# Performance work log

Measured on AMD Instinct MI355X. Metric: run time of the kernel, lower is better.

Reference implementation:

```python
import jax, jax.numpy as jnp
import numpy as np

D = 128  # head dim

def setup_inputs() -> dict:
    key = jax.random.key(0)
    k1, k2, k3, k4, k5 = jax.random.split(key, 5)
    B, N, M, C1, C2 = 4, 4096, 4096, 1024, 1024
    x = jax.random.normal(k1, (B, N, C1), dtype=jnp.float32)
    y = jax.random.normal(k2, (B, M, C2), dtype=jnp.float32)
    # Linear(c, d, bias=False): out = inp @ W where W is [c, d]
    Wq = jax.random.normal(k3, (C1, D), dtype=jnp.float32) / np.sqrt(C1)
    Wk = jax.random.normal(k4, (C2, D), dtype=jnp.float32) / np.sqrt(C2)
    Wv = jax.random.normal(k5, (C2, D), dtype=jnp.float32) / np.sqrt(C2)
    return {"x": x, "y": y, "Wq": Wq, "Wk": Wk, "Wv": Wv}

def reference(x, y, Wq, Wk, Wv):
    q = x @ Wq                               # [B, N, d]
    k = y @ Wk                               # [B, M, d]
    v = y @ Wv                               # [B, M, d]
    scale = 1.0 / jnp.sqrt(jnp.asarray(D, dtype=q.dtype))
    a = jnp.einsum('bnd,bmd->bnm', q, k) * scale
    a = jax.nn.softmax(a, axis=-1)           # softmax FIRST
    a = jnp.triu(a, k=1)                     # post-softmax causal mask (keeps strict upper)
    out = jnp.einsum('bnm,bmd->bnd', a, v)   # [B, N, d]
    return out
```

## Files before the change

kernel.cpp:

```cpp
#include <hip/hip_runtime.h>
#include <hip/hip_bf16.h>
#include <stdint.h>


typedef __attribute__((ext_vector_type(8))) __bf16    bf16x8;
typedef __attribute__((ext_vector_type(4))) float     floatx4;
typedef __attribute__((ext_vector_type(8))) uint16_t  u16x8;
typedef __attribute__((ext_vector_type(4))) uint32_t  u32x4;

#define DEVFN __device__ __forceinline__

DEVFN uint16_t f32_to_bf16(float f) {
  uint32_t u = __builtin_bit_cast(uint32_t, f);
  u += 0x7FFFu + ((u >> 16) & 1u);
  return (uint16_t)(u >> 16);
}

DEVFN uint32_t bcast(float f) { return __builtin_bit_cast(uint32_t, f); }

DEVFN uint32_t pack2_bf16(float a, float b) {
  return ((bcast(a) + 0x8000u) >> 16) | ((bcast(b) + 0x8000u) & 0xFFFF0000u);
}

DEVFN u32x4 pack_bf16_8(float4 a0, float4 a1) {
  u32x4 o;
  o[0] = pack2_bf16(a0.x, a0.y);
  o[1] = pack2_bf16(a0.z, a0.w);
  o[2] = pack2_bf16(a1.x, a1.y);
  o[3] = pack2_bf16(a1.z, a1.w);
  return o;
}

DEVFN void gl2lds16(const void* g, void* l) {
  __builtin_amdgcn_global_load_lds(
      (const __attribute__((address_space(1))) void*)g,
      (__attribute__((address_space(3))) void*)l, 16, 0, 0);
}

__global__ __launch_bounds__(256) void wt_kernel(
    const float* __restrict__ Wq, const float* __restrict__ Wk,
    const float* __restrict__ Wv, uint16_t* __restrict__ wt) {
  int tid = blockIdx.x * 256 + threadIdx.x;
  int mat = tid >> 14;
  int rem = tid & 16383;
  int n  = rem & 127;
  int k0 = rem >> 7;
  const float* W = (mat == 0) ? Wq : ((mat == 1) ? Wk : Wv);
  u16x8 v;
#pragma unroll
  for (int j = 0; j < 8; ++j) v[j] = f32_to_bf16(W[(k0 * 8 + j) * 128 + n]);
  *(u16x8*)&wt[mat * (128 * 1024) + n * 1024 + k0 * 8] = v;
}

__global__ __launch_bounds__(256, 3) void qkv_kernel(
    const float* __restrict__ x, const float* __restrict__ y,
    const uint16_t* __restrict__ wt, uint16_t* __restrict__ q,
    uint16_t* __restrict__ k, uint16_t* __restrict__ vt) {
  constexpr int AB = 8192;
  constexpr int WB = 16384;
  __shared__ __align__(16) uint8_t sA[2 * AB];
  __shared__ __align__(16) uint8_t sW[2 * WB];
  const int t = threadIdx.x;
  const int mat = blockIdx.y, rt = blockIdx.x;
  const float* A = (mat == 0) ? x : y;
  const uint16_t* Wt = wt + mat * (128 * 1024);
  const int lane = t & 63, wv = t >> 6;
  const int wr = wv >> 1, wc = wv & 1;
  const int cidx = lane & 15, quad = lane >> 4;
  const int Arow0 = rt * 64;

  const int ar  = t >> 2;
  const int acq = t & 3;
  const float* aptr = &A[(size_t)(Arow0 + ar) * 1024 + acq * 16];
  const int aw0 = ar * 128 + (((2 * acq) ^ (ar & 7)) * 16);
  const int aw1 = ar * 128 + (((2 * acq + 1) ^ (ar & 7)) * 16);

  int wsrc[4], wdst[4];
#pragma unroll
  for (int i = 0; i < 4; ++i) {
    int G = i * 256 + t;
    int n = G >> 3, g = G & 7;
    wsrc[i] = n * 1024 + ((g ^ (n & 7)) * 8);
    wdst[i] = G * 16;
  }

  floatx4 acc[2][4];
#pragma unroll
  for (int rg = 0; rg < 2; ++rg)
#pragma unroll
    for (int ng = 0; ng < 4; ++ng) acc[rg][ng] = (floatx4){0.f, 0.f, 0.f, 0.f};

  float4 f4[4], g4[4];

#pragma unroll
  for (int i = 0; i < 4; ++i)
    gl2lds16(Wt + wsrc[i], sW + wdst[i]);
#pragma unroll
  for (int j = 0; j < 4; ++j) f4[j] = *(const float4*)(aptr + j * 4);

  for (int kt = 0; kt < 16; ++kt) {
    const int cur = kt & 1, nxt = cur ^ 1;
    if (kt < 15) {
      const int kc = (kt + 1) * 64;
#pragma unroll
      for (int i = 0; i < 4; ++i)
        gl2lds16(Wt + kc + wsrc[i], sW + nxt * WB + wdst[i]);
#pragma unroll
      for (int j = 0; j < 4; ++j) g4[j] = *(const float4*)(aptr + kc + j * 4);
      __builtin_amdgcn_sched_barrier(0);
      asm volatile("s_waitcnt vmcnt(8)" ::: "memory");
    } else {
      __builtin_amdgcn_sched_barrier(0);
      asm volatile("s_waitcnt vmcnt(0)" ::: "memory");
    }
    __builtin_amdgcn_sched_barrier(0);

    *(u32x4*)(sA + cur * AB + aw0) = pack_bf16_8(f4[0], f4[1]);
    *(u32x4*)(sA + cur * AB + aw1) = pack_bf16_8(f4[2], f4[3]);
    __builtin_amdgcn_sched_barrier(0);
    asm volatile("s_waitcnt lgkmcnt(0)" ::: "memory");
    __builtin_amdgcn_s_barrier();
    __builtin_amdgcn_sched_barrier(0);

    bf16x8 af[2][2];
#pragma unroll
    for (int rg = 0; rg < 2; ++rg)
#pragma unroll
      for (int ks = 0; ks < 2; ++ks)
        af[rg][ks] = *(const bf16x8*)
            (sA + cur * AB + (wr * 32 + rg * 16 + cidx) * 128 +
             (((ks * 4 + quad) ^ (cidx & 7)) * 16));
    __builtin_amdgcn_s_setprio(1);
#pragma unroll
    for (int ng = 0; ng < 4; ++ng) {
      const int n = wc * 64 + ng * 16 + cidx;
      bf16x8 b0 = *(const bf16x8*)
          (sW + cur * WB + n * 128 + (((quad) ^ (cidx & 7)) * 16));
      bf16x8 b1 = *(const bf16x8*)
          (sW + cur * WB + n * 128 + (((4 + quad) ^ (cidx & 7)) * 16));
#pragma unroll
      for (int rg = 0; rg < 2; ++rg) {
        acc[rg][ng] = __builtin_amdgcn_mfma_f32_16x16x32_bf16(af[rg][0], b0, acc[rg][ng], 0, 0, 0);
        acc[rg][ng] = __builtin_amdgcn_mfma_f32_16x16x32_bf16(af[rg][1], b1, acc[rg][ng], 0, 0, 0);
      }
    }
    __builtin_amdgcn_s_setprio(0);
    __builtin_amdgcn_sched_barrier(0);
    asm volatile("s_waitcnt lgkmcnt(0)" ::: "memory");
    __builtin_amdgcn_s_barrier();
    __builtin_amdgcn_sched_barrier(0);

    if (kt < 15) {
#pragma unroll
      for (int j = 0; j < 4; ++j) f4[j] = g4[j];
    }
  }

  if (mat < 2) {
    uint16_t* outp = (mat == 0) ? q : k;
#pragma unroll
    for (int rg = 0; rg < 2; ++rg)
#pragma unroll
      for (int r = 0; r < 4; ++r) {
        int row = Arow0 + wr * 32 + rg * 16 + quad * 4 + r;
#pragma unroll
        for (int ng = 0; ng < 4; ++ng)
          outp[row * 128 + wc * 64 + ng * 16 + cidx] = f32_to_bf16(acc[rg][ng][r]);
      }
  } else {
    int bq = rt >> 6;
    int mbase = (rt & 63) * 64;
#pragma unroll
    for (int rg = 0; rg < 2; ++rg)
#pragma unroll
      for (int r = 0; r < 4; ++r) {
        int m = mbase + wr * 32 + rg * 16 + quad * 4 + r;
#pragma unroll
        for (int ng = 0; ng < 4; ++ng)
          vt[(size_t)(bq * 128 + wc * 64 + ng * 16 + cidx) * 4096 + m] =
              f32_to_bf16(acc[rg][ng][r]);
      }
  }
}

__global__ __launch_bounds__(256, 2) void attn_kernel(
    const uint16_t* __restrict__ q, const uint16_t* __restrict__ k,
    const uint16_t* __restrict__ vt, float* __restrict__ opart,
    float* __restrict__ lpart, int mlen, int iters) {
  constexpr int KB = 16384, VB = 16384;
  __shared__ __align__(16) uint8_t sK[2 * KB];
  __shared__ __align__(16) uint8_t sV[2 * VB];
  const int t = threadIdx.x;
  const int lane = t & 63, wv = t >> 6;
  const int cidx = lane & 15, quad = lane >> 4;
  const int qt = blockIdx.x, h = blockIdx.y, b = blockIdx.z;
  const int qmin = qt * 128 + wv * 32;
  const int mbase = h * mlen;

  const uint16_t* qb = q + (size_t)(b * 4096) * 128;
  const uint8_t* kb = (const uint8_t*)(k + (size_t)(b * 4096) * 128);
  const uint8_t* vb = (const uint8_t*)(vt + (size_t)(b * 128) * 4096);

  const float SC = 0.12751744610657223f;

  int kOffL[4], vOffL[4], kLds[4], vLds[4];
#pragma unroll
  for (int u = 0; u < 4; ++u) {
    int r  = wv * 16 + u * 4 + (lane >> 4);
    int g  = (lane & 15) ^ (r & 15);
    kOffL[u] = r * 256 + g * 16;
    kLds[u]  = (wv * 16 + u * 4) * 256;
    int rv = wv * 32 + u * 8 + (lane >> 3);
    int gv = (lane & 7) ^ (rv & 7);
    vOffL[u] = rv * 8192 + gv * 16;
    vLds[u]  = (wv * 32 + u * 8) * 128;
  }

  bf16x8 qf[2][4];
#pragma unroll
  for (int qg = 0; qg < 2; ++qg)
#pragma unroll
    for (int ks = 0; ks < 4; ++ks)
      qf[qg][ks] = *(const bf16x8*)
          &qb[(qmin + qg * 16 + cidx) * 128 + ks * 32 + quad * 8];

  floatx4 O[2][8];
#pragma unroll
  for (int qg = 0; qg < 2; ++qg)
#pragma unroll
    for (int dg = 0; dg < 8; ++dg) O[qg][dg] = (floatx4){0.f, 0.f, 0.f, 0.f};
  float lsum[2] = {0.f, 0.f};

#pragma unroll
  for (int u = 0; u < 4; ++u) {
    gl2lds16(kb + (size_t)mbase * 256 + kOffL[u], sK + kLds[u]);
    gl2lds16(vb + (size_t)mbase * 2 + vOffL[u], sV + vLds[u]);
  }
  __syncthreads();

  for (int it = 0; it < iters; ++it) {
    const int m0 = mbase + it * 64;
    const int cur = it & 1, nxt = cur ^ 1;
    if (it + 1 < iters) {
      const int m1 = m0 + 64;
#pragma unroll
      for (int u = 0; u < 4; ++u) {
        gl2lds16(kb + (size_t)m1 * 256 + kOffL[u], sK + nxt * KB + kLds[u]);
        gl2lds16(vb + (size_t)m1 * 2 + vOffL[u], sV + nxt * VB + vLds[u]);
      }
    }

    floatx4 accST[2][4];
#pragma unroll
    for (int qg = 0; qg < 2; ++qg)
#pragma unroll
      for (int ng = 0; ng < 4; ++ng) accST[qg][ng] = (floatx4){0.f, 0.f, 0.f, 0.f};
    __builtin_amdgcn_s_setprio(1);
#pragma unroll
    for (int ks = 0; ks < 4; ++ks)
#pragma unroll
      for (int ng = 0; ng < 4; ++ng) {
        bf16x8 kf = *(const bf16x8*)
            (sK + cur * KB + (ng * 16 + cidx) * 256 + ((ks * 4 + quad) ^ cidx) * 16);
        accST[0][ng] = __builtin_amdgcn_mfma_f32_16x16x32_bf16(kf, qf[0][ks], accST[0][ng], 0, 0, 0);
        accST[1][ng] = __builtin_amdgcn_mfma_f32_16x16x32_bf16(kf, qf[1][ks], accST[1][ng], 0, 0, 0);
      }
    __builtin_amdgcn_s_setprio(0);

    float p[2][4][4];
#pragma unroll
    for (int qg = 0; qg < 2; ++qg)
#pragma unroll
      for (int ng = 0; ng < 4; ++ng)
#pragma unroll
        for (int r = 0; r < 4; ++r) {
          p[qg][ng][r] = exp2f(accST[qg][ng][r] * SC);
          lsum[qg] += p[qg][ng][r];
        }

    if (m0 + 63 > qmin) {
#pragma unroll
      for (int qg = 0; qg < 2; ++qg) {
        const int base = qmin + qg * 16;
        if (m0 < base + 16) {
#pragma unroll
          for (int ng = 0; ng < 4; ++ng)
#pragma unroll
            for (int r = 0; r < 4; ++r) {
              int m = m0 + ng * 16 + quad * 4 + r;
              int n = base + cidx;
              if (m <= n) p[qg][ng][r] = 0.f;
            }
        }
      }
      uint32_t pk[2][4][2];
#pragma unroll
      for (int qg = 0; qg < 2; ++qg)
#pragma unroll
        for (int ng = 0; ng < 4; ++ng) {
          pk[qg][ng][0] = pack2_bf16(p[qg][ng][0], p[qg][ng][1]);
          pk[qg][ng][1] = pack2_bf16(p[qg][ng][2], p[qg][ng][3]);
        }
#pragma unroll
      for (int ks = 0; ks < 2; ++ks) {
        bf16x8 pbv[2];
#pragma unroll
        for (int qg = 0; qg < 2; ++qg) {
          u32x4 pbw;
#pragma unroll
          for (int j2 = 0; j2 < 4; ++j2) {
            int lr = ((quad & 1) << 3) + 2 * j2;
            int srcl = ((lr >> 2) << 4) + cidx;
            uint32_t lo = (uint32_t)__shfl((int)pk[qg][2 * ks][j2 & 1], srcl);
            uint32_t hi = (uint32_t)__shfl((int)pk[qg][2 * ks + 1][j2 & 1], srcl);
            pbw[j2] = (quad & 2) ? hi : lo;
          }
          pbv[qg] = __builtin_bit_cast(bf16x8, pbw);
        }
        __builtin_amdgcn_s_setprio(1);
#pragma unroll
        for (int dg = 0; dg < 8; ++dg) {
          bf16x8 vf = *(const bf16x8*)
              (sV + cur * VB + (dg * 16 + cidx) * 128 +
               (((ks * 4 + quad) ^ cidx) & 7) * 16);
          O[0][dg] = __builtin_amdgcn_mfma_f32_16x16x32_bf16(vf, pbv[0], O[0][dg], 0, 0, 0);
          O[1][dg] = __builtin_amdgcn_mfma_f32_16x16x32_bf16(vf, pbv[1], O[1][dg], 0, 0, 0);
        }
        __builtin_amdgcn_s_setprio(0);
      }
    }
    __syncthreads();
  }

#pragma unroll
  for (int qg = 0; qg < 2; ++qg) {
    lsum[qg] += __shfl_xor(lsum[qg], 16);
    lsum[qg] += __shfl_xor(lsum[qg], 32);
    const int n = qmin + qg * 16 + cidx;
    float* op = opart + ((size_t)h * 16384 + b * 4096 + n) * 128;
#pragma unroll
    for (int dg = 0; dg < 8; ++dg)
      *(float4*)&op[dg * 16 + quad * 4] = __builtin_bit_cast(float4, O[qg][dg]);
    if (quad == 0) lpart[h * 16384 + b * 4096 + n] = lsum[qg];
  }
}

__global__ __launch_bounds__(256) void combine_kernel(
    const float* __restrict__ opart, const float* __restrict__ lpart,
    float* __restrict__ out, int hcount) {
  size_t i = (size_t)blockIdx.x * 256 + threadIdx.x;
  size_t e = i * 4;
  int row = (int)(e >> 7);
  float4 acc = {0.f, 0.f, 0.f, 0.f};
  float l = 0.f;
  for (int h = 0; h < hcount; ++h) {
    float4 ov = *(const float4*)&opart[(size_t)h * 2097152 + e];
    acc.x += ov.x; acc.y += ov.y; acc.z += ov.z; acc.w += ov.w;
    l += lpart[h * 16384 + row];
  }
  float inv = 1.0f / l;
  float4 o;
  o.x = acc.x * inv; o.y = acc.y * inv; o.z = acc.z * inv; o.w = acc.w * inv;
  *(float4*)&out[e] = o;
}

extern "C" void kernel_launch(void* const* d_in, const int* in_sizes, int n_in,
                              void* d_out, int out_size, void* d_ws, size_t ws_size,
                              hipStream_t stream) {
  const float* x  = (const float*)d_in[0];
  const float* y  = (const float*)d_in[1];
  const float* Wq = (const float*)d_in[2];
  const float* Wk = (const float*)d_in[3];
  const float* Wv = (const float*)d_in[4];
  uint16_t* ws = (uint16_t*)d_ws;
  uint16_t* wt = ws;
  uint16_t* q  = ws + 393216;
  uint16_t* k  = q + 2097152;
  uint16_t* vt = k + 2097152;
  float* opart = (float*)((char*)d_ws + 13369344);
  int hcount = (ws_size >= (size_t)13369344 + 4 * 8454144) ? 4 : 2;
  float* lpart = opart + (size_t)hcount * 2097152;
  float* o = (float*)d_out;
  int mlen = 4096 / hcount, iters = mlen / 64;

  hipLaunchKernelGGL(wt_kernel,      dim3(192),            dim3(256), 0, stream, Wq, Wk, Wv, wt);
  hipLaunchKernelGGL(qkv_kernel,     dim3(256, 3),         dim3(256), 0, stream, x, y, wt, q, k, vt);
  hipLaunchKernelGGL(attn_kernel,    dim3(32, hcount, 4),  dim3(256), 0, stream, q, k, vt, opart, lpart, mlen, iters);
  hipLaunchKernelGGL(combine_kernel, dim3(2048),           dim3(256), 0, stream, opart, lpart, o, hcount);
}
```

Measured before the change: 230.1 us.

## Prefetch projection tiles two stages ahead through registers instead of direct LDS loads

```diff
diff --git a/kernel.cpp b/kernel.cpp
--- a/kernel.cpp
+++ b/kernel.cpp
@@ -80,8 +80,8 @@
   for (int i = 0; i < 4; ++i) {
     int G = i * 256 + t;
     int n = G >> 3, g = G & 7;
-    wsrc[i] = n * 1024 + ((g ^ (n & 7)) * 8);
-    wdst[i] = G * 16;
+    wsrc[i] = n * 1024 + g * 8;
+    wdst[i] = n * 128 + ((g ^ (n & 7)) * 16);
   }
 
   floatx4 acc[2][4];
@@ -90,71 +90,82 @@
 #pragma unroll
     for (int ng = 0; ng < 4; ++ng) acc[rg][ng] = (floatx4){0.f, 0.f, 0.f, 0.f};
 
-  float4 f4[4], g4[4];
-
-#pragma unroll
-  for (int i = 0; i < 4; ++i)
-    gl2lds16(Wt + wsrc[i], sW + wdst[i]);
-#pragma unroll
-  for (int j = 0; j < 4; ++j) f4[j] = *(const float4*)(aptr + j * 4);
-
-  for (int kt = 0; kt < 16; ++kt) {
-    const int cur = kt & 1, nxt = cur ^ 1;
-    if (kt < 15) {
-      const int kc = (kt + 1) * 64;
-#pragma unroll
-      for (int i = 0; i < 4; ++i)
-        gl2lds16(Wt + kc + wsrc[i], sW + nxt * WB + wdst[i]);
-#pragma unroll
-      for (int j = 0; j < 4; ++j) g4[j] = *(const float4*)(aptr + kc + j * 4);
-      __builtin_amdgcn_sched_barrier(0);
-      asm volatile("s_waitcnt vmcnt(8)" ::: "memory");
-    } else {
-      __builtin_amdgcn_sched_barrier(0);
-      asm volatile("s_waitcnt vmcnt(0)" ::: "memory");
-    }
-    __builtin_amdgcn_sched_barrier(0);
-
-    *(u32x4*)(sA + cur * AB + aw0) = pack_bf16_8(f4[0], f4[1]);
-    *(u32x4*)(sA + cur * AB + aw1) = pack_bf16_8(f4[2], f4[3]);
-    __builtin_amdgcn_sched_barrier(0);
-    asm volatile("s_waitcnt lgkmcnt(0)" ::: "memory");
-    __builtin_amdgcn_s_barrier();
-    __builtin_amdgcn_sched_barrier(0);
-
-    bf16x8 af[2][2];
-#pragma unroll
-    for (int rg = 0; rg < 2; ++rg)
-#pragma unroll
-      for (int ks = 0; ks < 2; ++ks)
-        af[rg][ks] = *(const bf16x8*)
-            (sA + cur * AB + (wr * 32 + rg * 16 + cidx) * 128 +
-             (((ks * 4 + quad) ^ (cidx & 7)) * 16));
-    __builtin_amdgcn_s_setprio(1);
-#pragma unroll
-    for (int ng = 0; ng < 4; ++ng) {
-      const int n = wc * 64 + ng * 16 + cidx;
-      bf16x8 b0 = *(const bf16x8*)
-          (sW + cur * WB + n * 128 + (((quad) ^ (cidx & 7)) * 16));
-      bf16x8 b1 = *(const bf16x8*)
-          (sW + cur * WB + n * 128 + (((4 + quad) ^ (cidx & 7)) * 16));
-#pragma unroll
-      for (int rg = 0; rg < 2; ++rg) {
-        acc[rg][ng] = __builtin_amdgcn_mfma_f32_16x16x32_bf16(af[rg][0], b0, acc[rg][ng], 0, 0, 0);
-        acc[rg][ng] = __builtin_amdgcn_mfma_f32_16x16x32_bf16(af[rg][1], b1, acc[rg][ng], 0, 0, 0);
-      }
-    }
-    __builtin_amdgcn_s_setprio(0);
-    __builtin_amdgcn_sched_barrier(0);
-    asm volatile("s_waitcnt lgkmcnt(0)" ::: "memory");
-    __builtin_amdgcn_s_barrier();
-    __builtin_amdgcn_sched_barrier(0);
-
-    if (kt < 15) {
-#pragma unroll
-      for (int j = 0; j < 4; ++j) f4[j] = g4[j];
-    }
-  }
+  float4 fa[4], fb[4];
+  u16x8  wa[4], wb[4];
+
+#pragma unroll
+  for (int j = 0; j < 4; ++j) fa[j] = *(const float4*)(aptr + j * 4);
+#pragma unroll
+  for (int i = 0; i < 4; ++i) wa[i] = *(const u16x8*)&Wt[wsrc[i]];
+#pragma unroll
+  for (int j = 0; j < 4; ++j) fb[j] = *(const float4*)(aptr + 64 + j * 4);
+#pragma unroll
+  for (int i = 0; i < 4; ++i) wb[i] = *(const u16x8*)&Wt[wsrc[i] + 64];
+  __builtin_amdgcn_sched_barrier(0);
+  asm volatile("s_waitcnt vmcnt(8)" ::: "memory");
+  __builtin_amdgcn_sched_barrier(0);
+  *(u32x4*)(sA + aw0) = pack_bf16_8(fa[0], fa[1]);
+  *(u32x4*)(sA + aw1) = pack_bf16_8(fa[2], fa[3]);
+#pragma unroll
+  for (int i = 0; i < 4; ++i) *(u16x8*)(sW + wdst[i]) = wa[i];
+  __builtin_amdgcn_sched_barrier(0);
+  asm volatile("s_waitcnt lgkmcnt(0)" ::: "memory");
+  __builtin_amdgcn_s_barrier();
+  __builtin_amdgcn_sched_barrier(0);
+
+#define QSTEP(KT, CURF, CURW, OTHF, OTHW, P)                                  \
+  {                                                                           \
+    if ((KT) + 2 < 16) {                                                      \
+      const int kc = ((KT) + 2) * 64;                                         \
+      _Pragma("unroll") for (int j = 0; j < 4; ++j)                           \
+          CURF[j] = *(const float4*)(aptr + kc + j * 4);                      \
+      _Pragma("unroll") for (int i = 0; i < 4; ++i)                           \
+          CURW[i] = *(const u16x8*)&Wt[wsrc[i] + kc];                         \
+    }                                                                         \
+    __builtin_amdgcn_sched_barrier(0);                                        \
+    if ((KT) + 2 < 16) { asm volatile("s_waitcnt vmcnt(8)" ::: "memory"); }   \
+    else               { asm volatile("s_waitcnt vmcnt(0)" ::: "memory"); }   \
+    __builtin_amdgcn_sched_barrier(0);                                        \
+    if ((KT) + 1 < 16) {                                                      \
+      *(u32x4*)(sA + ((P) ^ 1) * AB + aw0) = pack_bf16_8(OTHF[0], OTHF[1]);   \
+      *(u32x4*)(sA + ((P) ^ 1) * AB + aw1) = pack_bf16_8(OTHF[2], OTHF[3]);   \
+      _Pragma("unroll") for (int i = 0; i < 4; ++i)                           \
+          *(u16x8*)(sW + ((P) ^ 1) * WB + wdst[i]) = OTHW[i];                 \
+    }                                                                         \
+    __builtin_amdgcn_sched_barrier(0);                                        \
+    asm volatile("s_waitcnt lgkmcnt(0)" ::: "memory");                        \
+    __builtin_amdgcn_s_barrier();                                             \
+    __builtin_amdgcn_sched_barrier(0);                                        \
+    bf16x8 af[2][2];                                                          \
+    _Pragma("unroll") for (int rg = 0; rg < 2; ++rg)                          \
+      _Pragma("unroll") for (int ks = 0; ks < 2; ++ks)                        \
+        af[rg][ks] = *(const bf16x8*)                                         \
+            (sA + (P) * AB + (wr * 32 + rg * 16 + cidx) * 128 +               \
+             (((ks * 4 + quad) ^ (cidx & 7)) * 16));                          \
+    __builtin_amdgcn_s_setprio(1);                                            \
+    _Pragma("unroll") for (int ng = 0; ng < 4; ++ng) {                        \
+      const int n = wc * 64 + ng * 16 + cidx;                                 \
+      bf16x8 b0 = *(const bf16x8*)                                            \
+          (sW + (P) * WB + n * 128 + (((quad) ^ (cidx & 7)) * 16));           \
+      bf16x8 b1 = *(const bf16x8*)                                            \
+          (sW + (P) * WB + n * 128 + (((4 + quad) ^ (cidx & 7)) * 16));       \
+      _Pragma("unroll") for (int rg = 0; rg < 2; ++rg) {                      \
+        acc[rg][ng] = __builtin_amdgcn_mfma_f32_16x16x32_bf16(af[rg][0], b0, acc[rg][ng], 0, 0, 0); \
+        acc[rg][ng] = __builtin_amdgcn_mfma_f32_16x16x32_bf16(af[rg][1], b1, acc[rg][ng], 0, 0, 0); \
+      }                                                                       \
+    }                                                                         \
+    __builtin_amdgcn_s_setprio(0);                                            \
+    __builtin_amdgcn_sched_barrier(0);                                        \
+    asm volatile("s_waitcnt lgkmcnt(0)" ::: "memory");                        \
+    __builtin_amdgcn_s_barrier();                                             \
+    __builtin_amdgcn_sched_barrier(0);                                        \
+  }
+
+  for (int kt2 = 0; kt2 < 16; kt2 += 2) {
+    QSTEP(kt2,     fa, wa, fb, wb, 0);
+    QSTEP(kt2 + 1, fb, wb, fa, wa, 1);
+  }
+#undef QSTEP
 
   if (mat < 2) {
     uint16_t* outp = (mat == 0) ? q : k;
```

After: 239.5 us. 1.04x slower.
